# Kernel optimization log

Measured on AMD Instinct MI355X. Metric: run time of the kernel, lower is better.

Reference implementation:

```python
import jax, jax.numpy as jnp
import numpy as np

DN = ('NCHW', 'OIHW', 'NCHW')
COMMITMENT = 0.25


def conv(x, w, b, s, p):
    y = jax.lax.conv_general_dilated(x, w, (s, s), ((p, p), (p, p)), dimension_numbers=DN)
    return y + b[None, :, None, None]


def deconv(x, w, b, s, p, op):
    # PyTorch ConvTranspose2d(w: [in,out,kh,kw]) == dilated conv with flipped, transposed kernel
    k = w.shape[2]
    w2 = jnp.flip(jnp.transpose(w, (1, 0, 2, 3)), (2, 3))  # -> [out,in,kh,kw]
    pad = ((k - 1 - p, k - 1 - p + op), (k - 1 - p, k - 1 - p + op))
    y = jax.lax.conv_general_dilated(x, w2, (1, 1), pad, lhs_dilation=(s, s), dimension_numbers=DN)
    return y + b[None, :, None, None]


def setup_inputs():
    key = jax.random.key(0)
    ks = jax.random.split(key, 14)
    g = lambda k, shp: jax.random.normal(k, shp, jnp.float32) * 0.05
    x = jax.random.uniform(ks[0], (128, 3, 128, 128), dtype=jnp.float32)
    return {
        'x': x,
        'enc_w1': g(ks[1], (32, 3, 4, 4)), 'enc_b1': jnp.zeros((32,), jnp.float32),
        'enc_w2': g(ks[2], (64, 32, 4, 4)), 'enc_b2': jnp.zeros((64,), jnp.float32),
        'enc_w3': g(ks[3], (64, 64, 4, 4)), 'enc_b3': jnp.zeros((64,), jnp.float32),
        'codebook': jax.random.uniform(ks[4], (512, 64), jnp.float32, -1.0 / 512, 1.0 / 512),
        'dec_w1': g(ks[5], (64, 64, 4, 4)), 'dec_b1': jnp.zeros((64,), jnp.float32),
        'dec_w2': g(ks[6], (64, 32, 4, 4)), 'dec_b2': jnp.zeros((32,), jnp.float32),
        'dec_w3': g(ks[7], (32, 3, 4, 4)), 'dec_b3': jnp.zeros((3,), jnp.float32),
    }


def reference(x, enc_w1, enc_b1, enc_w2, enc_b2, enc_w3, enc_b3, codebook,
              dec_w1, dec_b1, dec_w2, dec_b2, dec_w3, dec_b3):
    sg = jax.lax.stop_gradient
    # encoder: 128 -> 64 -> 32 -> 16
    h = jax.nn.relu(conv(x, enc_w1, enc_b1, 2, 1))
    h = jax.nn.relu(conv(h, enc_w2, enc_b2, 2, 1))
    z = conv(h, enc_w3, enc_b3, 2, 1)  # [B, 64, 16, 16]
    B, C, H, W = z.shape
    zf = jnp.transpose(z, (0, 2, 3, 1)).reshape(-1, C)  # [N, 64]
    # squared-distance: ||z||^2 + ||e||^2 - 2 z e^T
    d = (jnp.sum(zf * zf, axis=1, keepdims=True)
         + jnp.sum(codebook * codebook, axis=1)
         - 2.0 * zf @ codebook.T)  # [N, 512]
    idx = jnp.argmin(d, axis=1)  # [N]
    q = codebook[idx]  # gather == onehot @ codebook
    e_latent = jnp.mean((sg(q) - zf) ** 2)
    q_latent = jnp.mean((q - sg(zf)) ** 2)
    vq_loss = q_latent + COMMITMENT * e_latent
    qst = zf + sg(q - zf)  # straight-through
    z_q = jnp.transpose(qst.reshape(B, H, W, C), (0, 3, 1, 2))
    # decoder: 16 -> 32 -> 64 -> 131 (last layer: p=0, output_padding=1)
    h = jax.nn.relu(deconv(z_q, dec_w1, dec_b1, 2, 1, 0))
    h = jax.nn.relu(deconv(h, dec_w2, dec_b2, 2, 1, 0))
    x_recon = jax.nn.sigmoid(deconv(h, dec_w3, dec_b3, 2, 0, 1))
    return x_recon, vq_loss, idx[:, None]
```

## Files before the change

kernel.cpp:

```cpp
#include <hip/hip_runtime.h>


template<typename F>
__device__ __forceinline__ float pairwise64_sq(F get)
{
    float r[8];
    #pragma unroll
    for (int j = 0; j < 8; ++j) {
        const float v = get(j);
        r[j] = __fmul_rn(v, v);
    }
    #pragma unroll
    for (int b = 1; b < 8; ++b)
        #pragma unroll
        for (int j = 0; j < 8; ++j) {
            const float v = get(8 * b + j);
            r[j] = __fadd_rn(r[j], __fmul_rn(v, v));
        }
    return __fadd_rn(__fadd_rn(__fadd_rn(r[0], r[1]), __fadd_rn(r[2], r[3])),
                     __fadd_rn(__fadd_rn(r[4], r[5]), __fadd_rn(r[6], r[7])));
}

template<int CIN, int COUT, int HIN, int TOH, int ICC, bool RELU>
__global__ void __launch_bounds__(256)
conv_s2(const float* __restrict__ x, const float* __restrict__ w,
        const float* __restrict__ bias, float* __restrict__ y)
{
    constexpr int WIN = HIN, HOUT = HIN / 2, WOUT = WIN / 2;
    constexpr int NOWG = WOUT / 4, NOCG = COUT / 4;
    static_assert(TOH * NOWG * NOCG == 256, "block mismatch");
    static_assert(CIN % ICC == 0, "chunking mismatch");
    constexpr int NCH = CIN / ICC;
    constexpr int NIR = 2 * TOH + 2;
    constexpr int LW  = WIN + 2;
    constexpr int SWP = ICC * 16 + 1;

    __shared__ float sx[ICC][NIR][LW];
    __shared__ float sw[COUT][SWP];

    const int n   = blockIdx.x;
    const int oh0 = blockIdx.y * TOH;
    const int t   = threadIdx.x;
    const int owg = t % NOWG;
    const int ohl = (t / NOWG) % TOH;
    const int ocg = t / (NOWG * TOH);
    const int oh  = oh0 + ohl;
    const int ow0 = owg * 4;
    const int ih0 = 2 * oh0 - 1;

    float acc[4][4];
    #pragma unroll
    for (int i = 0; i < 4; ++i)
        #pragma unroll
        for (int j = 0; j < 4; ++j) acc[i][j] = 0.f;

    for (int ch = 0; ch < NCH; ++ch) {
        const int ic0 = ch * ICC;
        for (int idx = t; idx < COUT * ICC * 16; idx += 256) {
            const int k   = idx & 15;
            const int icl = (idx >> 4) % ICC;
            const int oc  = idx / (16 * ICC);
            sw[oc][icl * 16 + k] = w[(oc * CIN + ic0 + icl) * 16 + k];
        }
        for (int idx = t; idx < ICC * NIR * LW; idx += 256) {
            const int c   = idx % LW;
            const int r   = (idx / LW) % NIR;
            const int icl = idx / (LW * NIR);
            const int ih  = ih0 + r;
            const int iw  = c - 1;
            float v = 0.f;
            if (ih >= 0 && ih < HIN && iw >= 0 && iw < WIN)
                v = x[((size_t)(n * CIN + ic0 + icl) * HIN + ih) * WIN + iw];
            sx[icl][r][c] = v;
        }
        __syncthreads();
        #pragma unroll
        for (int icl = 0; icl < ICC; ++icl) {
            float in[4][10];
            #pragma unroll
            for (int kh = 0; kh < 4; ++kh)
                #pragma unroll
                for (int c = 0; c < 10; ++c)
                    in[kh][c] = sx[icl][2 * ohl + kh][2 * ow0 + c];
            #pragma unroll
            for (int ol = 0; ol < 4; ++ol) {
                const int oc = ocg * 4 + ol;
                #pragma unroll
                for (int kh = 0; kh < 4; ++kh)
                    #pragma unroll
                    for (int kw = 0; kw < 4; ++kw) {
                        const float wv = sw[oc][icl * 16 + kh * 4 + kw];
                        #pragma unroll
                        for (int j = 0; j < 4; ++j)
                            acc[ol][j] = __fmaf_rn(in[kh][2 * j + kw], wv,
                                                   acc[ol][j]);
                    }
            }
        }
        __syncthreads();
    }
    #pragma unroll
    for (int ol = 0; ol < 4; ++ol) {
        const int oc = ocg * 4 + ol;
        const float bv = bias[oc];
        float r0 = __fadd_rn(acc[ol][0], bv), r1 = __fadd_rn(acc[ol][1], bv);
        float r2 = __fadd_rn(acc[ol][2], bv), r3 = __fadd_rn(acc[ol][3], bv);
        if (RELU) {
            r0 = fmaxf(r0, 0.f); r1 = fmaxf(r1, 0.f);
            r2 = fmaxf(r2, 0.f); r3 = fmaxf(r3, 0.f);
        }
        float4* o = reinterpret_cast<float4*>(
            &y[((size_t)(n * COUT + oc) * HOUT + oh) * WOUT + ow0]);
        *o = make_float4(r0, r1, r2, r3);
    }
}

template<int CIN, int COUT, int HIN, int TOH, int ICC, bool RELU>
__global__ void __launch_bounds__(256)
deconv_s2(const float* __restrict__ x, const float* __restrict__ w,
          const float* __restrict__ bias, float* __restrict__ y)
{
    constexpr int WIN = HIN, HOUT = 2 * HIN, WOUT = 2 * WIN;
    constexpr int NOWG = WOUT / 4, NOCG = COUT / 4;
    static_assert(TOH * NOWG * NOCG == 256, "block mismatch");
    static_assert(CIN % ICC == 0, "chunking mismatch");
    static_assert(TOH == 2, "row-tile fixed at 2");
    constexpr int NCH = CIN / ICC;
    constexpr int NIR = 3;
    constexpr int LW  = WIN + 2;

    __shared__ float sx[ICC][NIR][LW];
    __shared__ float sw[ICC][COUT][17];

    const int n   = blockIdx.x;
    const int oh0 = blockIdx.y * TOH;
    const int t   = threadIdx.x;
    const int owg = t % NOWG;
    const int ohl = (t / NOWG) % TOH;
    const int ocg = t / (NOWG * TOH);
    const int oh  = oh0 + ohl;
    const int ow0 = owg * 4;
    const int ih0 = oh0 / 2 - 1;
    const int p1  = (oh + 1) & 1;
    const int r1  = ((oh + 1) >> 1) - ih0;

    float acc[4][4];
    #pragma unroll
    for (int i = 0; i < 4; ++i)
        #pragma unroll
        for (int j = 0; j < 4; ++j) acc[i][j] = 0.f;

    for (int ch = 0; ch < NCH; ++ch) {
        const int ic0 = ch * ICC;
        for (int idx = t; idx < ICC * COUT * 16; idx += 256) {
            const int k   = idx & 15;
            const int co  = (idx >> 4) % COUT;
            const int icl = idx / (16 * COUT);
            sw[icl][co][k] = w[((size_t)(ic0 + icl) * COUT + co) * 16 + k];
        }
        for (int idx = t; idx < ICC * NIR * LW; idx += 256) {
            const int c   = idx % LW;
            const int r   = (idx / LW) % NIR;
            const int icl = idx / (LW * NIR);
            const int ih  = ih0 + r;
            const int iw  = c - 1;
            float v = 0.f;
            if (ih >= 0 && ih < HIN && iw >= 0 && iw < WIN)
                v = x[((size_t)(n * CIN + ic0 + icl) * HIN + ih) * WIN + iw];
            sx[icl][r][c] = v;
        }
        __syncthreads();
        #pragma unroll
        for (int icl = 0; icl < ICC; ++icl) {
            float xv[2][4];
            #pragma unroll
            for (int rr = 0; rr < 2; ++rr)
                #pragma unroll
                for (int c = 0; c < 4; ++c)
                    xv[rr][c] = sx[icl][r1 - 1 + rr][ow0 / 2 + c];
            #pragma unroll
            for (int ol = 0; ol < 4; ++ol) {
                const int co = ocg * 4 + ol;
                float wv[2][4];
                #pragma unroll
                for (int a = 0; a < 2; ++a)
                    #pragma unroll
                    for (int kw = 0; kw < 4; ++kw)
                        wv[a][kw] = sw[icl][co][(p1 + 2 * a) * 4 + kw];
                acc[ol][0] += xv[1][1]*wv[0][1] + xv[0][1]*wv[1][1]
                            + xv[1][0]*wv[0][3] + xv[0][0]*wv[1][3];
                acc[ol][1] += xv[1][2]*wv[0][0] + xv[0][2]*wv[1][0]
                            + xv[1][1]*wv[0][2] + xv[0][1]*wv[1][2];
                acc[ol][2] += xv[1][2]*wv[0][1] + xv[0][2]*wv[1][1]
                            + xv[1][1]*wv[0][3] + xv[0][1]*wv[1][3];
                acc[ol][3] += xv[1][3]*wv[0][0] + xv[0][3]*wv[1][0]
                            + xv[1][2]*wv[0][2] + xv[0][2]*wv[1][2];
            }
        }
        __syncthreads();
    }
    #pragma unroll
    for (int ol = 0; ol < 4; ++ol) {
        const int co = ocg * 4 + ol;
        const float bv = bias[co];
        float r0 = acc[ol][0] + bv, r1 = acc[ol][1] + bv;
        float r2 = acc[ol][2] + bv, r3 = acc[ol][3] + bv;
        if (RELU) {
            r0 = fmaxf(r0, 0.f); r1 = fmaxf(r1, 0.f);
            r2 = fmaxf(r2, 0.f); r3 = fmaxf(r3, 0.f);
        }
        float4* o = reinterpret_cast<float4*>(
            &y[((size_t)(n * COUT + co) * HOUT + oh) * WOUT + ow0]);
        *o = make_float4(r0, r1, r2, r3);
    }
}

__global__ void __launch_bounds__(256)
deconv3_sig(const float* __restrict__ x, const float* __restrict__ w,
            const float* __restrict__ bias, float* __restrict__ y)
{
    __shared__ float sx[32][2][64];
    __shared__ float sw[32][3][16];
    const int n = blockIdx.x;
    const int r = blockIdx.y;
    const int t = threadIdx.x;

    float* swf = &sw[0][0][0];
    for (int idx = t; idx < 32 * 3 * 16; idx += 256) swf[idx] = w[idx];
    for (int idx = t; idx < 32 * 2 * 64; idx += 256) {
        const int c  = idx & 63;
        const int rr = (idx >> 6) & 1;
        const int ci = idx >> 7;
        const int ih = r - 1 + rr;
        sx[ci][rr][c] = (ih >= 0 && ih < 64)
            ? x[((size_t)(n * 32 + ci) * 64 + ih) * 64 + c] : 0.f;
    }
    __syncthreads();
    const float b0 = bias[0], b1 = bias[1], b2 = bias[2];
    for (int p = t; p < 262; p += 256) {
        const int dh = p / 131;
        const int oh = 2 * r + dh;
        if (oh >= 131) continue;
        const int ow  = p - dh * 131;
        const int kh1 = oh & 1, kw1 = ow & 1;
        const int c1  = ow >> 1;
        const int c2  = c1 - 1;
        const bool v1 = (c1 < 64);
        const bool v2 = (c2 >= 0 && c2 < 64);
        float a0 = 0.f, a1 = 0.f, a2 = 0.f;
        const int w11 = kh1 * 4 + kw1;
        const int w21 = (kh1 + 2) * 4 + kw1;
        const int w12 = kh1 * 4 + kw1 + 2;
        const int w22 = (kh1 + 2) * 4 + kw1 + 2;
        #pragma unroll 8
        for (int ci = 0; ci < 32; ++ci) {
            const float x11 = v1 ? sx[ci][1][c1] : 0.f;
            const float x01 = v1 ? sx[ci][0][c1] : 0.f;
            const float x10 = v2 ? sx[ci][1][c2] : 0.f;
            const float x00 = v2 ? sx[ci][0][c2] : 0.f;
            a0 = fmaf(x11, sw[ci][0][w11], a0); a0 = fmaf(x01, sw[ci][0][w21], a0);
            a0 = fmaf(x10, sw[ci][0][w12], a0); a0 = fmaf(x00, sw[ci][0][w22], a0);
            a1 = fmaf(x11, sw[ci][1][w11], a1); a1 = fmaf(x01, sw[ci][1][w21], a1);
            a1 = fmaf(x10, sw[ci][1][w12], a1); a1 = fmaf(x00, sw[ci][1][w22], a1);
            a2 = fmaf(x11, sw[ci][2][w11], a2); a2 = fmaf(x01, sw[ci][2][w21], a2);
            a2 = fmaf(x10, sw[ci][2][w12], a2); a2 = fmaf(x00, sw[ci][2][w22], a2);
        }
        const size_t base = (size_t)n * 3 * 17161 + (size_t)oh * 131 + ow;
        y[base]             = 1.0f / (1.0f + expf(-(a0 + b0)));
        y[base + 17161]     = 1.0f / (1.0f + expf(-(a1 + b1)));
        y[base + 2 * 17161] = 1.0f / (1.0f + expf(-(a2 + b2)));
    }
}

__global__ void __launch_bounds__(256)
esum_np_kernel(const float* __restrict__ cb, float* __restrict__ esum)
{
    const int j = blockIdx.x * 256 + threadIdx.x;
    if (j < 512) {
        const float* row = cb + j * 64;
        esum[j] = pairwise64_sq([&](int c) { return row[c]; });
    }
}

__global__ void __launch_bounds__(256)
vq_kernel_np(const float* __restrict__ z, const float* __restrict__ cb,
             const float* __restrict__ esum, float* __restrict__ zq,
             float* __restrict__ oidx, float* __restrict__ oloss)
{
    __shared__ float scb[64][64];
    __shared__ float red[128];
    const int t  = threadIdx.x;
    const int i  = blockIdx.x * 128 + (t >> 1);
    const int cs = (t & 1) * 32;
    const int n  = i >> 8;
    const int hw = i & 255;
    const float* zb = z + (size_t)n * 16384 + hw;

    float zr[64];
    #pragma unroll
    for (int c = 0; c < 64; ++c) zr[c] = zb[(size_t)c * 256];

    const float zz = pairwise64_sq([&](int c) { return zr[c]; });

    float best = 3.4e38f;
    int bi = 0;
    float* scf = &scb[0][0];
    for (int ch = 0; ch < 8; ++ch) {
        __syncthreads();
        for (int idx2 = t; idx2 < 4096; idx2 += 256)
            scf[idx2] = cb[ch * 4096 + idx2];
        __syncthreads();
        #pragma unroll 1
        for (int j4 = 0; j4 < 32; j4 += 4) {
            const float4* p0 = reinterpret_cast<const float4*>(&scb[cs + j4 + 0][0]);
            const float4* p1 = reinterpret_cast<const float4*>(&scb[cs + j4 + 1][0]);
            const float4* p2 = reinterpret_cast<const float4*>(&scb[cs + j4 + 2][0]);
            const float4* p3 = reinterpret_cast<const float4*>(&scb[cs + j4 + 3][0]);
            float a0 = 0.f, a1 = 0.f, a2 = 0.f, a3 = 0.f;
            #pragma unroll
            for (int c4 = 0; c4 < 16; ++c4) {
                const float4 v0 = p0[c4];
                const float4 v1 = p1[c4];
                const float4 v2 = p2[c4];
                const float4 v3 = p3[c4];
                const int c = c4 * 4;
                a0 = __fmaf_rn(zr[c+0], v0.x, a0);
                a0 = __fmaf_rn(zr[c+1], v0.y, a0);
                a0 = __fmaf_rn(zr[c+2], v0.z, a0);
                a0 = __fmaf_rn(zr[c+3], v0.w, a0);
                a1 = __fmaf_rn(zr[c+0], v1.x, a1);
                a1 = __fmaf_rn(zr[c+1], v1.y, a1);
                a1 = __fmaf_rn(zr[c+2], v1.z, a1);
                a1 = __fmaf_rn(zr[c+3], v1.w, a1);
                a2 = __fmaf_rn(zr[c+0], v2.x, a2);
                a2 = __fmaf_rn(zr[c+1], v2.y, a2);
                a2 = __fmaf_rn(zr[c+2], v2.z, a2);
                a2 = __fmaf_rn(zr[c+3], v2.w, a2);
                a3 = __fmaf_rn(zr[c+0], v3.x, a3);
                a3 = __fmaf_rn(zr[c+1], v3.y, a3);
                a3 = __fmaf_rn(zr[c+2], v3.z, a3);
                a3 = __fmaf_rn(zr[c+3], v3.w, a3);
            }
            const int base = ch * 64 + cs + j4;
            const float d0 = __fsub_rn(__fadd_rn(zz, esum[base + 0]),
                                       __fmul_rn(2.0f, a0));
            const float d1 = __fsub_rn(__fadd_rn(zz, esum[base + 1]),
                                       __fmul_rn(2.0f, a1));
            const float d2 = __fsub_rn(__fadd_rn(zz, esum[base + 2]),
                                       __fmul_rn(2.0f, a2));
            const float d3 = __fsub_rn(__fadd_rn(zz, esum[base + 3]),
                                       __fmul_rn(2.0f, a3));
            if (d0 < best) { best = d0; bi = base + 0; }
            if (d1 < best) { best = d1; bi = base + 1; }
            if (d2 < best) { best = d2; bi = base + 2; }
            if (d3 < best) { best = d3; bi = base + 3; }
        }
    }
    {
        const float ob  = __shfl_xor(best, 1);
        const int   obi = __shfl_xor(bi, 1);
        if (ob < best || (ob == best && obi < bi)) { best = ob; bi = obi; }
    }
    if ((t & 1) == 0) {
        const float* e = cb + (size_t)bi * 64;
        float rs = 0.f;
        #pragma unroll
        for (int c = 0; c < 64; ++c) {
            const float qv = e[c];
            const float df = qv - zr[c];
            rs = fmaf(df, df, rs);
            zq[((size_t)n * 64 + c) * 256 + hw] = zr[c] + (qv - zr[c]);
        }
        oidx[i] = (float)bi;
        red[t >> 1] = rs;
    }
    __syncthreads();
    for (int s = 64; s > 0; s >>= 1) {
        if (t < s) red[t] += red[t + s];
        __syncthreads();
    }
    if (t == 0)
        atomicAdd(oloss, red[0] * (1.25f / (32768.0f * 64.0f)));
}

extern "C" void kernel_launch(void* const* d_in, const int* in_sizes, int n_in,
                              void* d_out, int out_size, void* d_ws, size_t ws_size,
                              hipStream_t stream)
{
    (void)in_sizes; (void)n_in; (void)out_size; (void)ws_size;
    const float* x   = (const float*)d_in[0];
    const float* ew1 = (const float*)d_in[1];
    const float* eb1 = (const float*)d_in[2];
    const float* ew2 = (const float*)d_in[3];
    const float* eb2 = (const float*)d_in[4];
    const float* ew3 = (const float*)d_in[5];
    const float* eb3 = (const float*)d_in[6];
    const float* cb  = (const float*)d_in[7];
    const float* dw1 = (const float*)d_in[8];
    const float* db1 = (const float*)d_in[9];
    const float* dw2 = (const float*)d_in[10];
    const float* db2 = (const float*)d_in[11];
    const float* dw3 = (const float*)d_in[12];
    const float* db3 = (const float*)d_in[13];
    float* out = (float*)d_out;
    float* ws  = (float*)d_ws;

    float* h1 = ws;
    float* h2 = h1 + 16777216;
    float* z  = h2 + 8388608;
    float* zq = z  + 2097152;
    float* es = zq + 2097152;
    float* d1 = h2;
    float* d2 = h1;

    constexpr size_t RECON = (size_t)128 * 3 * 131 * 131;

    conv_s2<3, 32, 128, 2, 3, true ><<<dim3(128, 32), 256, 0, stream>>>(x,  ew1, eb1, h1);
    conv_s2<32, 64,  64, 2, 8, true ><<<dim3(128, 16), 256, 0, stream>>>(h1, ew2, eb2, h2);
    conv_s2<64, 64,  32, 4, 8, false><<<dim3(128,  4), 256, 0, stream>>>(h2, ew3, eb3, z);

    esum_np_kernel<<<dim3(2), 256, 0, stream>>>(cb, es);
    hipMemsetAsync(out + RECON, 0, sizeof(float), stream);
    vq_kernel_np<<<dim3(256), 256, 0, stream>>>(z, cb, es, zq,
                                                out + RECON + 1, out + RECON);

    deconv_s2<64, 64, 16, 2, 8, true><<<dim3(128, 16), 256, 0, stream>>>(zq, dw1, db1, d1);
    deconv_s2<64, 32, 32, 2, 8, true><<<dim3(128, 32), 256, 0, stream>>>(d1, dw2, db2, d2);
    deconv3_sig<<<dim3(128, 66), 256, 0, stream>>>(d2, dw3, db3, out);
}
```

Before: 1.171 ms.

## Enlarge deconv register tile to 8 outputs x 4 channels with vectorized LDS loads

Replaces the stride-2 deconvolution kernel with a version where each thread computes 8 output columns for 4 output channels and a block covers 4 output rows instead of 2. Shared-memory input and weight tiles are padded so they can be read with float4/float2 loads, and weights are staged with float4 global loads. The larger tile raises arithmetic per LDS load and halves the grid, but uses more registers and shared memory, which may lower occupancy.

```diff
diff --git a/kernel.cpp b/kernel.cpp
--- a/kernel.cpp
+++ b/kernel.cpp
@@ -115,54 +115,54 @@
     }
 }
 
-template<int CIN, int COUT, int HIN, int TOH, int ICC, bool RELU>
+template<int CIN, int COUT, int HIN, int ICC, bool RELU>
 __global__ void __launch_bounds__(256)
-deconv_s2(const float* __restrict__ x, const float* __restrict__ w,
-          const float* __restrict__ bias, float* __restrict__ y)
+deconv_s2_v2(const float* __restrict__ x, const float* __restrict__ w,
+             const float* __restrict__ bias, float* __restrict__ y)
 {
     constexpr int WIN = HIN, HOUT = 2 * HIN, WOUT = 2 * WIN;
-    constexpr int NOWG = WOUT / 4, NOCG = COUT / 4;
-    static_assert(TOH * NOWG * NOCG == 256, "block mismatch");
+    constexpr int NOW8 = WOUT / 8, NOC4 = COUT / 4;
+    static_assert(NOW8 * NOC4 * 4 == 256, "block mismatch");
     static_assert(CIN % ICC == 0, "chunking mismatch");
-    static_assert(TOH == 2, "row-tile fixed at 2");
     constexpr int NCH = CIN / ICC;
-    constexpr int NIR = 3;
-    constexpr int LW  = WIN + 2;
-
-    __shared__ float sx[ICC][NIR][LW];
-    __shared__ float sw[ICC][COUT][17];
+    constexpr int LW  = (WIN + 2 + 3) & ~3;
+    constexpr int SWP = 20;
+
+    __shared__ float sx[ICC][4][LW];
+    __shared__ float sw[ICC][COUT][SWP];
 
     const int n   = blockIdx.x;
-    const int oh0 = blockIdx.y * TOH;
+    const int oh0 = blockIdx.y * 4;
     const int t   = threadIdx.x;
-    const int owg = t % NOWG;
-    const int ohl = (t / NOWG) % TOH;
-    const int ocg = t / (NOWG * TOH);
-    const int oh  = oh0 + ohl;
-    const int ow0 = owg * 4;
-    const int ih0 = oh0 / 2 - 1;
+    const int owg = t % NOW8;
+    const int ocg = (t / NOW8) % NOC4;
+    const int oq  = t / (NOW8 * NOC4);
+    const int oh  = oh0 + oq;
+    const int ihb = oh0 / 2 - 1;
     const int p1  = (oh + 1) & 1;
-    const int r1  = ((oh + 1) >> 1) - ih0;
-
-    float acc[4][4];
+    const int r1  = ((oh + 1) >> 1) - ihb;
+
+    float acc[4][8];
     #pragma unroll
     for (int i = 0; i < 4; ++i)
         #pragma unroll
-        for (int j = 0; j < 4; ++j) acc[i][j] = 0.f;
+        for (int j = 0; j < 8; ++j) acc[i][j] = 0.f;
 
     for (int ch = 0; ch < NCH; ++ch) {
         const int ic0 = ch * ICC;
-        for (int idx = t; idx < ICC * COUT * 16; idx += 256) {
-            const int k   = idx & 15;
-            const int co  = (idx >> 4) % COUT;
-            const int icl = idx / (16 * COUT);
-            sw[icl][co][k] = w[((size_t)(ic0 + icl) * COUT + co) * 16 + k];
-        }
-        for (int idx = t; idx < ICC * NIR * LW; idx += 256) {
+        for (int idx = t; idx < ICC * COUT * 4; idx += 256) {
+            const int k4  = idx & 3;
+            const int co  = (idx >> 2) % COUT;
+            const int icl = idx / (4 * COUT);
+            const float4 v = reinterpret_cast<const float4*>(w)
+                                [((size_t)(ic0 + icl) * COUT + co) * 4 + k4];
+            *reinterpret_cast<float4*>(&sw[icl][co][k4 * 4]) = v;
+        }
+        for (int idx = t; idx < ICC * 4 * LW; idx += 256) {
             const int c   = idx % LW;
-            const int r   = (idx / LW) % NIR;
-            const int icl = idx / (LW * NIR);
-            const int ih  = ih0 + r;
+            const int r   = (idx / LW) & 3;
+            const int icl = idx / (LW * 4);
+            const int ih  = ihb + r;
             const int iw  = c - 1;
             float v = 0.f;
             if (ih >= 0 && ih < HIN && iw >= 0 && iw < WIN)
@@ -172,46 +172,47 @@
         __syncthreads();
         #pragma unroll
         for (int icl = 0; icl < ICC; ++icl) {
-            float xv[2][4];
+            float xv0[6], xv1[6];
+            {
+                const float4 a = *reinterpret_cast<const float4*>(&sx[icl][r1 - 1][owg * 4]);
+                const float2 b = *reinterpret_cast<const float2*>(&sx[icl][r1 - 1][owg * 4 + 4]);
+                xv0[0] = a.x; xv0[1] = a.y; xv0[2] = a.z; xv0[3] = a.w;
+                xv0[4] = b.x; xv0[5] = b.y;
+                const float4 c4 = *reinterpret_cast<const float4*>(&sx[icl][r1][owg * 4]);
+                const float2 d  = *reinterpret_cast<const float2*>(&sx[icl][r1][owg * 4 + 4]);
+                xv1[0] = c4.x; xv1[1] = c4.y; xv1[2] = c4.z; xv1[3] = c4.w;
+                xv1[4] = d.x;  xv1[5] = d.y;
+            }
             #pragma unroll
-            for (int rr = 0; rr < 2; ++rr)
-                #pragma unroll
-                for (int c = 0; c < 4; ++c)
-                    xv[rr][c] = sx[icl][r1 - 1 + rr][ow0 / 2 + c];
-            #pragma unroll
-            for (int ol = 0; ol < 4; ++ol) {
-                const int co = ocg * 4 + ol;
-                float wv[2][4];
-                #pragma unroll
-                for (int a = 0; a < 2; ++a)
-                    #pragma unroll
-                    for (int kw = 0; kw < 4; ++kw)
-                        wv[a][kw] = sw[icl][co][(p1 + 2 * a) * 4 + kw];
-                acc[ol][0] += xv[1][1]*wv[0][1] + xv[0][1]*wv[1][1]
-                            + xv[1][0]*wv[0][3] + xv[0][0]*wv[1][3];
-                acc[ol][1] += xv[1][2]*wv[0][0] + xv[0][2]*wv[1][0]
-                            + xv[1][1]*wv[0][2] + xv[0][1]*wv[1][2];
-                acc[ol][2] += xv[1][2]*wv[0][1] + xv[0][2]*wv[1][1]
-                            + xv[1][1]*wv[0][3] + xv[0][1]*wv[1][3];
-                acc[ol][3] += xv[1][3]*wv[0][0] + xv[0][3]*wv[1][0]
-                            + xv[1][2]*wv[0][2] + xv[0][2]*wv[1][2];
+            for (int cl = 0; cl < 4; ++cl) {
+                const int co = ocg * 4 + cl;
+                const float4 w0 = *reinterpret_cast<const float4*>(&sw[icl][co][p1 * 4]);
+                const float4 w1 = *reinterpret_cast<const float4*>(&sw[icl][co][(p1 + 2) * 4]);
+                acc[cl][0] += xv1[1]*w0.y + xv0[1]*w1.y + xv1[0]*w0.w + xv0[0]*w1.w;
+                acc[cl][1] += xv1[2]*w0.x + xv0[2]*w1.x + xv1[1]*w0.z + xv0[1]*w1.z;
+                acc[cl][2] += xv1[2]*w0.y + xv0[2]*w1.y + xv1[1]*w0.w + xv0[1]*w1.w;
+                acc[cl][3] += xv1[3]*w0.x + xv0[3]*w1.x + xv1[2]*w0.z + xv0[2]*w1.z;
+                acc[cl][4] += xv1[3]*w0.y + xv0[3]*w1.y + xv1[2]*w0.w + xv0[2]*w1.w;
+                acc[cl][5] += xv1[4]*w0.x + xv0[4]*w1.x + xv1[3]*w0.z + xv0[3]*w1.z;
+                acc[cl][6] += xv1[4]*w0.y + xv0[4]*w1.y + xv1[3]*w0.w + xv0[3]*w1.w;
+                acc[cl][7] += xv1[5]*w0.x + xv0[5]*w1.x + xv1[4]*w0.z + xv0[4]*w1.z;
             }
         }
         __syncthreads();
     }
     #pragma unroll
-    for (int ol = 0; ol < 4; ++ol) {
-        const int co = ocg * 4 + ol;
+    for (int cl = 0; cl < 4; ++cl) {
+        const int co = ocg * 4 + cl;
         const float bv = bias[co];
-        float r0 = acc[ol][0] + bv, r1 = acc[ol][1] + bv;
-        float r2 = acc[ol][2] + bv, r3 = acc[ol][3] + bv;
-        if (RELU) {
-            r0 = fmaxf(r0, 0.f); r1 = fmaxf(r1, 0.f);
-            r2 = fmaxf(r2, 0.f); r3 = fmaxf(r3, 0.f);
-        }
-        float4* o = reinterpret_cast<float4*>(
-            &y[((size_t)(n * COUT + co) * HOUT + oh) * WOUT + ow0]);
-        *o = make_float4(r0, r1, r2, r3);
+        float r[8];
+        #pragma unroll
+        for (int j = 0; j < 8; ++j) {
+            r[j] = acc[cl][j] + bv;
+            if (RELU) r[j] = fmaxf(r[j], 0.f);
+        }
+        float* o = &y[((size_t)(n * COUT + co) * HOUT + oh) * WOUT + owg * 8];
+        *reinterpret_cast<float4*>(o)     = make_float4(r[0], r[1], r[2], r[3]);
+        *reinterpret_cast<float4*>(o + 4) = make_float4(r[4], r[5], r[6], r[7]);
     }
 }
 
@@ -424,7 +425,7 @@
     vq_kernel_np<<<dim3(256), 256, 0, stream>>>(z, cb, es, zq,
                                                 out + RECON + 1, out + RECON);
 
-    deconv_s2<64, 64, 16, 2, 8, true><<<dim3(128, 16), 256, 0, stream>>>(zq, dw1, db1, d1);
-    deconv_s2<64, 32, 32, 2, 8, true><<<dim3(128, 32), 256, 0, stream>>>(d1, dw2, db2, d2);
+    deconv_s2_v2<64, 64, 16,  8, true><<<dim3(128,  8), 256, 0, stream>>>(zq, dw1, db1, d1);
+    deconv_s2_v2<64, 32, 32, 16, true><<<dim3(128, 16), 256, 0, stream>>>(d1, dw2, db2, d2);
     deconv3_sig<<<dim3(128, 66), 256, 0, stream>>>(d2, dw3, db3, out);
 }
```

Result: slower. 1.453 ms (+24.1%).
